# Optimization experiments

Measured on AMD Instinct MI355X. Metric: run time of the kernel, lower is better.

Reference implementation:

```python
import jax, jax.numpy as jnp
import numpy as np

# ---- fan-beam geometry config (uniform path: no pmatrix, uniform SID/SDD/angle/offcenter) ----
SID = 750.0          # source-to-isocenter distance (mm)
SDD = 1250.0         # source-to-detector distance (mm)
VIEWS = 128          # number of projection angles
NDET = 512           # detector element count
DET_ELT = 1.2        # detector element size (mm)
DET_OFF = 0.0        # detector offcenter (mm)
START_ANGLE = 0.0    # degrees
TOTAL_ANGLE = 360.0  # degrees
IMG_DIM = 256        # image is IMG_DIM x IMG_DIM
PIX = 1.0            # pixel size (mm)
STEP = 1.0           # fpjStepSize: ray sampling step (mm)
R = IMG_DIM * PIX * np.sqrt(2.0) / 2.0   # half image diagonal: ray segment to sample
NS = int(np.ceil(2.0 * R / STEP)) + 1    # samples per ray (static)


def _sample_points():
    # Per-view source / detector geometry; rays sampled from t = SID-R to SID+R.
    beta = jnp.asarray(np.deg2rad(START_ANGLE + TOTAL_ANGLE * np.arange(VIEWS) / VIEWS),
                       jnp.float32)                                    # [V]
    cb, sb = jnp.cos(beta), jnp.sin(beta)
    src = SID * jnp.stack([cb, sb], -1)                                 # [V,2] source position
    det0 = src - SDD * jnp.stack([cb, sb], -1)                          # [V,2] detector center
    eu = jnp.stack([-sb, cb], -1)                                       # [V,2] detector tangent
    u = (jnp.arange(NDET, dtype=jnp.float32) - (NDET - 1) / 2.0) * DET_ELT + DET_OFF  # [N]
    det = det0[:, None, :] + u[None, :, None] * eu[:, None, :]          # [V,N,2]
    d = det - src[:, None, :]
    d = d / jnp.linalg.norm(d, axis=-1, keepdims=True)                  # unit ray directions
    t = SID - R + STEP * jnp.arange(NS, dtype=jnp.float32)              # [NS]
    pts = src[:, None, None, :] + t[None, None, :, None] * d[:, :, None, :]  # [V,N,NS,2]
    return pts


def setup_inputs() -> dict:
    key = jax.random.key(0)
    x = jax.random.uniform(key, (2, IMG_DIM, IMG_DIM), dtype=jnp.float32)  # attenuation image batch
    return {"x": x}


def reference(x):
    # Ray-driven fan-beam forward projection: line integral via bilinear sampling.
    pts = _sample_points()                      # [V,N,NS,2] world coords (mm)
    px, py = pts[..., 0], pts[..., 1]
    jx = px / PIX + (IMG_DIM - 1) / 2.0         # continuous column index
    iy = (IMG_DIM - 1) / 2.0 - py / PIX         # continuous row index (y up)
    j0f = jnp.floor(jx)
    i0f = jnp.floor(iy)
    fj = jx - j0f
    fi = iy - i0f
    i0 = i0f.astype(jnp.int32)
    j0 = j0f.astype(jnp.int32)

    def gather(ii, jj):
        valid = (ii >= 0) & (ii < IMG_DIM) & (jj >= 0) & (jj < IMG_DIM)
        ic = jnp.clip(ii, 0, IMG_DIM - 1)
        jc = jnp.clip(jj, 0, IMG_DIM - 1)
        return x[:, ic, jc] * valid[None].astype(x.dtype)   # [B,V,N,NS]

    v00 = gather(i0, j0)
    v01 = gather(i0, j0 + 1)
    v10 = gather(i0 + 1, j0)
    v11 = gather(i0 + 1, j0 + 1)
    interp = (v00 * (1 - fi) * (1 - fj) + v01 * (1 - fi) * fj
              + v10 * fi * (1 - fj) + v11 * fi * fj)        # [B,V,N,NS]
    sinogram = interp.sum(-1) * STEP                        # [B,V,N]
    return sinogram
```

## Files before the change

kernel.cpp:

```cpp
#include <hip/hip_runtime.h>
#include <hip/hip_fp16.h>
#include <math.h>
#include <string.h>

constexpr int   VIEWS = 128;
constexpr int   NDET  = 512;
constexpr int   IMG   = 256;
constexpr int   BATCH = 2;
constexpr float SID_F = 750.0f;
constexpr float SDD_F = 1250.0f;
constexpr float DET_ELT = 1.2f;
constexpr float DET_OFF = 0.0f;
constexpr float STEP  = 1.0f;
constexpr int   NS = 364;
constexpr float T0 = (float)(750.0 - 181.01933598375618);

constexpr int PAD    = 2;
constexpr int TROWS  = IMG + 2 * PAD;
constexpr int TSTR   = 262;
constexpr int TWSTR  = TSTR / 2;
constexpr int TWORDS = TROWS * TWSTR;

typedef _Float16 h2 __attribute__((ext_vector_type(2)));
using v2h = decltype(__builtin_amdgcn_cvt_pkrtz(0.0f, 0.0f));

__global__ __launch_bounds__(1024) void fanbeam_lds(const float* __restrict__ img,
                                                    float* __restrict__ out) {
    __shared__ unsigned int tile32[TWORDS];
    __shared__ float red[1024];
    const int tid = threadIdx.x;
    const int blk = blockIdx.x;
    const int v = blk & (VIEWS - 1);
    const int b = blk >> 7;

    for (int k = tid; k < 524 + 768; k += 1024) {
        int w;
        if (k < 524) {
            const int r = k / 131, c = k - r * 131;
            const int row = (r < 2) ? r : 256 + r;
            w = row * TWSTR + c;
        } else {
            const int kk = k - 524;
            const int row = 2 + kk / 3;
            const int m = kk % 3;
            w = row * TWSTR + ((m == 0) ? 0 : 128 + m);
        }
        tile32[w] = 0u;
    }

    const float* __restrict__ src = img + b * IMG * IMG;
    for (int k = tid; k < (IMG * IMG) / 4; k += 1024) {
        const int p = k * 4;
        const int i = p >> 8;
        const int j = p & 255;
        const float4 f = *reinterpret_cast<const float4*>(src + p);
        const unsigned lo = ((unsigned)__half_as_ushort(__float2half(f.y)) << 16)
                          |  (unsigned)__half_as_ushort(__float2half(f.x));
        const unsigned hi = ((unsigned)__half_as_ushort(__float2half(f.w)) << 16)
                          |  (unsigned)__half_as_ushort(__float2half(f.z));
        const int h = (i + PAD) * TSTR + (j + PAD);
        tile32[h >> 1]       = lo;
        tile32[(h >> 1) + 1] = hi;
    }
    __syncthreads();

    const int n     = tid & (NDET - 1);
    const int chunk = tid >> 9;
    const float beta = (float)((double)v * 0.049087385212340517);
    const float cb = cosf(beta);
    const float sb = sinf(beta);
    const float u  = ((float)n - 255.5f) * DET_ELT + DET_OFF;
    float dx = fmaf(-u, sb, -SDD_F * cb);
    float dy = fmaf( u, cb, -SDD_F * sb);
    const float inv = rsqrtf(fmaf(dx, dx, dy * dy));
    dx *= inv;
    dy *= inv;
    const float ndy = -dy;
    const float sx = SID_F * cb;
    const float sy = SID_F * sb;
    const float cx3 = fmaf(T0, dx,  sx + 127.5f + (float)PAD);
    const float cy3 = fmaf(T0, ndy, 127.5f - sy + (float)PAD);

    const float invx = 1.0f / dx;
    const float invy = 1.0f / dy;
    const float ta = (-128.75f - sx) * invx, tb = (128.75f - sx) * invx;
    const float tc = (-128.75f - sy) * invy, td = (128.75f - sy) * invy;
    const float txmin = fminf(ta, tb), txmax = fmaxf(ta, tb);
    const float tymin = fminf(tc, td), tymax = fmaxf(tc, td);
    const float tmin = fmaxf(fmaxf(txmin, tymin), T0);
    const float tmax = fminf(fminf(txmax, tymax), T0 + (float)(NS - 1));
    int slo = (int)ceilf(tmin - T0);
    int shi = (int)floorf(tmax - T0);
    slo = max(slo, 0);
    shi = min(shi, NS - 1);

    float acc = 0.0f;
    const int start = slo + chunk;
    const int iters = max(0, (shi - start + 2) / 2);
    float sfv = (float)start;

#pragma unroll 4
    for (int k = 0; k < iters; ++k) {
        const float jx2 = fmaf(sfv, dx, cx3);
        const float iy2 = fmaf(sfv, ndy, cy3);
        sfv += 2.0f;
        const int jp = (int)jx2;
        const int ip = (int)iy2;
        const float fj = jx2 - (float)jp;
        const float fi = iy2 - (float)ip;
        const int w = ip * TWSTR + (jp >> 1);
        const unsigned w0 = tile32[w];
        const unsigned w1 = tile32[w + 1];
        const unsigned w2 = tile32[w + TWSTR];
        const unsigned w3 = tile32[w + TWSTR + 1];
        const unsigned sh = (unsigned)jp << 4;
        const unsigned ptop = __builtin_amdgcn_alignbit(w1, w0, sh);
        const unsigned pbot = __builtin_amdgcn_alignbit(w3, w2, sh);
        const unsigned Lu = __builtin_amdgcn_perm(pbot, ptop, 0x05040100u);
        const unsigned Hu = __builtin_amdgcn_perm(pbot, ptop, 0x07060302u);
        const h2 L = __builtin_bit_cast(h2, Lu);
        const h2 H = __builtin_bit_cast(h2, Hu);
        const h2 fj2 = __builtin_bit_cast(h2, __builtin_amdgcn_cvt_pkrtz(fj, fj));
        const h2 r = fj2 * (H - L) + L;
#if __has_builtin(__builtin_amdgcn_fdot2)
        const h2 wv = __builtin_bit_cast(h2, __builtin_amdgcn_cvt_pkrtz(1.0f - fi, fi));
        acc = __builtin_amdgcn_fdot2(__builtin_bit_cast(v2h, r),
                                     __builtin_bit_cast(v2h, wv), acc, false);
#else
        const float top = (float)r.x;
        const float bot = (float)r.y;
        acc = fmaf(fi, bot - top, acc + top);
#endif
    }

    red[tid] = acc;
    __syncthreads();
    if (tid < 512) {
        out[blk * 512 + tid] = (red[tid] + red[tid + 512]) * STEP;
    }
}

extern "C" void kernel_launch(void* const* d_in, const int* in_sizes, int n_in,
                              void* d_out, int out_size, void* d_ws, size_t ws_size,
                              hipStream_t stream) {
    const float* x = (const float*)d_in[0];
    float* out = (float*)d_out;
    fanbeam_lds<<<BATCH * VIEWS, 1024, 0, stream>>>(x, out);
}
```

Before: 77.02 us.

## Store vertically paired fp16 texels and process image in two row bands

Changes the LDS layout so each 32-bit word holds a pixel and the one below it. A bilinear sample then needs two LDS reads instead of four, and the alignbit/perm unpacking goes away. The doubled tile no longer fits for the whole image, so the image is loaded in two overlapping row bands, and each ray's sample range is split at the band boundary. The cost is a second tile load with scalar, uncoalesced-width global reads and fp16 conversion, plus extra barriers. Block-level memory-load latency is also no longer overlapped.

```diff
diff --git a/kernel.cpp b/kernel.cpp
--- a/kernel.cpp
+++ b/kernel.cpp
@@ -1,7 +1,6 @@
 #include <hip/hip_runtime.h>
 #include <hip/hip_fp16.h>
 #include <math.h>
-#include <string.h>
 
 constexpr int   VIEWS = 128;
 constexpr int   NDET  = 512;
@@ -15,54 +14,60 @@
 constexpr int   NS = 364;
 constexpr float T0 = (float)(750.0 - 181.01933598375618);
 
-constexpr int PAD    = 2;
-constexpr int TROWS  = IMG + 2 * PAD;
-constexpr int TSTR   = 262;
-constexpr int TWSTR  = TSTR / 2;
-constexpr int TWORDS = TROWS * TWSTR;
+constexpr int COLS  = 260;
+constexpr int CSTR  = 261;
+constexpr int SPLIT = 130;
+constexpr int NE_T  = 131;
+constexpr int NE_B  = 130;
+constexpr int BLO_B = 129;
 
 typedef _Float16 h2 __attribute__((ext_vector_type(2)));
 using v2h = decltype(__builtin_amdgcn_cvt_pkrtz(0.0f, 0.0f));
 
-__global__ __launch_bounds__(1024) void fanbeam_lds(const float* __restrict__ img,
-                                                    float* __restrict__ out) {
-    __shared__ unsigned int tile32[TWORDS];
+__device__ __forceinline__ float band_loop(const unsigned* __restrict__ tb,
+                                           int lo, int hi, int chunk,
+                                           float dx, float ndy,
+                                           float cx3, float cy3) {
+    float acc = 0.0f;
+    const int start = lo + chunk;
+    const int iters = max(0, (hi - start + 2) / 2);
+    float sfv = (float)start;
+#pragma unroll 4
+    for (int k = 0; k < iters; ++k) {
+        const float jx2 = fmaf(sfv, dx, cx3);
+        const float iy2 = fmaf(sfv, ndy, cy3);
+        sfv += 2.0f;
+        const int jp = (int)jx2;
+        const int ip = (int)iy2;
+        const float fj = jx2 - (float)jp;
+        const float fi = iy2 - (float)ip;
+        const int addr = ip * CSTR + jp;
+        const unsigned Lu = tb[addr];
+        const unsigned Hu = tb[addr + 1];
+        const h2 L = __builtin_bit_cast(h2, Lu);
+        const h2 H = __builtin_bit_cast(h2, Hu);
+        const h2 fj2 = __builtin_bit_cast(h2, __builtin_amdgcn_cvt_pkrtz(fj, fj));
+        const h2 r = fj2 * (H - L) + L;
+#if __has_builtin(__builtin_amdgcn_fdot2)
+        const h2 wv = __builtin_bit_cast(h2, __builtin_amdgcn_cvt_pkrtz(1.0f - fi, fi));
+        acc = __builtin_amdgcn_fdot2(__builtin_bit_cast(v2h, r),
+                                     __builtin_bit_cast(v2h, wv), acc, false);
+#else
+        acc = fmaf(fi, (float)r.y - (float)r.x, acc + (float)r.x);
+#endif
+    }
+    return acc;
+}
+
+__global__ __launch_bounds__(1024) void fanbeam_pair(const float* __restrict__ img,
+                                                     float* __restrict__ out) {
+    __shared__ unsigned tile[NE_T * CSTR];
     __shared__ float red[1024];
     const int tid = threadIdx.x;
     const int blk = blockIdx.x;
     const int v = blk & (VIEWS - 1);
     const int b = blk >> 7;
-
-    for (int k = tid; k < 524 + 768; k += 1024) {
-        int w;
-        if (k < 524) {
-            const int r = k / 131, c = k - r * 131;
-            const int row = (r < 2) ? r : 256 + r;
-            w = row * TWSTR + c;
-        } else {
-            const int kk = k - 524;
-            const int row = 2 + kk / 3;
-            const int m = kk % 3;
-            w = row * TWSTR + ((m == 0) ? 0 : 128 + m);
-        }
-        tile32[w] = 0u;
-    }
-
     const float* __restrict__ src = img + b * IMG * IMG;
-    for (int k = tid; k < (IMG * IMG) / 4; k += 1024) {
-        const int p = k * 4;
-        const int i = p >> 8;
-        const int j = p & 255;
-        const float4 f = *reinterpret_cast<const float4*>(src + p);
-        const unsigned lo = ((unsigned)__half_as_ushort(__float2half(f.y)) << 16)
-                          |  (unsigned)__half_as_ushort(__float2half(f.x));
-        const unsigned hi = ((unsigned)__half_as_ushort(__float2half(f.w)) << 16)
-                          |  (unsigned)__half_as_ushort(__float2half(f.z));
-        const int h = (i + PAD) * TSTR + (j + PAD);
-        tile32[h >> 1]       = lo;
-        tile32[(h >> 1) + 1] = hi;
-    }
-    __syncthreads();
 
     const int n     = tid & (NDET - 1);
     const int chunk = tid >> 9;
@@ -72,68 +77,74 @@
     const float u  = ((float)n - 255.5f) * DET_ELT + DET_OFF;
     float dx = fmaf(-u, sb, -SDD_F * cb);
     float dy = fmaf( u, cb, -SDD_F * sb);
-    const float inv = rsqrtf(fmaf(dx, dx, dy * dy));
-    dx *= inv;
-    dy *= inv;
+    const float rinv = rsqrtf(fmaf(dx, dx, dy * dy));
+    dx *= rinv;
+    dy *= rinv;
     const float ndy = -dy;
     const float sx = SID_F * cb;
     const float sy = SID_F * sb;
-    const float cx3 = fmaf(T0, dx,  sx + 127.5f + (float)PAD);
-    const float cy3 = fmaf(T0, ndy, 127.5f - sy + (float)PAD);
+    const float cx3 = fmaf(T0, dx,  sx + 127.5f + 2.0f);
+    const float cy3 = fmaf(T0, ndy, 127.5f - sy + 2.0f);
 
     const float invx = 1.0f / dx;
     const float invy = 1.0f / dy;
-    const float ta = (-128.75f - sx) * invx, tb = (128.75f - sx) * invx;
+    const float ta = (-128.75f - sx) * invx, tb2 = (128.75f - sx) * invx;
     const float tc = (-128.75f - sy) * invy, td = (128.75f - sy) * invy;
-    const float txmin = fminf(ta, tb), txmax = fmaxf(ta, tb);
-    const float tymin = fminf(tc, td), tymax = fmaxf(tc, td);
-    const float tmin = fmaxf(fmaxf(txmin, tymin), T0);
-    const float tmax = fminf(fminf(txmax, tymax), T0 + (float)(NS - 1));
+    const float tmin = fmaxf(fmaxf(fminf(ta, tb2), fminf(tc, td)), T0);
+    const float tmax = fminf(fminf(fmaxf(ta, tb2), fmaxf(tc, td)), T0 + (float)(NS - 1));
     int slo = (int)ceilf(tmin - T0);
     int shi = (int)floorf(tmax - T0);
     slo = max(slo, 0);
     shi = min(shi, NS - 1);
 
-    float acc = 0.0f;
-    const int start = slo + chunk;
-    const int iters = max(0, (shi - start + 2) / 2);
-    float sfv = (float)start;
+    float zf = (cy3 - (float)SPLIT) * invy;
+    zf = fminf(fmaxf(zf, -1.0e6f), 1.0e6f);
+    const int zc  = (int)ceilf(zf);
+    const int zfl = (int)floorf(zf);
 
-#pragma unroll 4
-    for (int k = 0; k < iters; ++k) {
-        const float jx2 = fmaf(sfv, dx, cx3);
-        const float iy2 = fmaf(sfv, ndy, cy3);
-        sfv += 2.0f;
-        const int jp = (int)jx2;
-        const int ip = (int)iy2;
-        const float fj = jx2 - (float)jp;
-        const float fi = iy2 - (float)ip;
-        const int w = ip * TWSTR + (jp >> 1);
-        const unsigned w0 = tile32[w];
-        const unsigned w1 = tile32[w + 1];
-        const unsigned w2 = tile32[w + TWSTR];
-        const unsigned w3 = tile32[w + TWSTR + 1];
-        const unsigned sh = (unsigned)jp << 4;
-        const unsigned ptop = __builtin_amdgcn_alignbit(w1, w0, sh);
-        const unsigned pbot = __builtin_amdgcn_alignbit(w3, w2, sh);
-        const unsigned Lu = __builtin_amdgcn_perm(pbot, ptop, 0x05040100u);
-        const unsigned Hu = __builtin_amdgcn_perm(pbot, ptop, 0x07060302u);
-        const h2 L = __builtin_bit_cast(h2, Lu);
-        const h2 H = __builtin_bit_cast(h2, Hu);
-        const h2 fj2 = __builtin_bit_cast(h2, __builtin_amdgcn_cvt_pkrtz(fj, fj));
-        const h2 r = fj2 * (H - L) + L;
-#if __has_builtin(__builtin_amdgcn_fdot2)
-        const h2 wv = __builtin_bit_cast(h2, __builtin_amdgcn_cvt_pkrtz(1.0f - fi, fi));
-        acc = __builtin_amdgcn_fdot2(__builtin_bit_cast(v2h, r),
-                                     __builtin_bit_cast(v2h, wv), acc, false);
-#else
-        const float top = (float)r.x;
-        const float bot = (float)r.y;
-        acc = fmaf(fi, bot - top, acc + top);
-#endif
+    for (int k = tid; k < NE_T * COLS; k += 1024) {
+        const int e = k / COLS;
+        const int j = k - e * COLS;
+        const int r0 = e - 2, r1 = e - 1, c = j - 2;
+        const bool cv = (unsigned)c < 256u;
+        unsigned plo = 0, phi = 0;
+        if (cv && (unsigned)r0 < 256u)
+            plo = __half_as_ushort(__float2half(src[(r0 << 8) + c]));
+        if (cv && (unsigned)r1 < 256u)
+            phi = __half_as_ushort(__float2half(src[(r1 << 8) + c]));
+        tile[e * CSTR + j] = plo | (phi << 16);
     }
+    __syncthreads();
+    int lo_, hi_;
+    if (ndy > 0.0f)      { lo_ = slo; hi_ = min(shi, zc - 1); }
+    else if (ndy < 0.0f) { lo_ = max(slo, zfl + 1); hi_ = shi; }
+    else                 { lo_ = (cy3 < (float)SPLIT) ? slo : 1;
+                           hi_ = (cy3 < (float)SPLIT) ? shi : 0; }
+    const float accT = band_loop(tile, lo_, hi_, chunk, dx, ndy, cx3, cy3);
+    __syncthreads();
 
-    red[tid] = acc;
+    for (int k = tid; k < NE_B * COLS; k += 1024) {
+        const int e = k / COLS;
+        const int j = k - e * COLS;
+        const int p = e + BLO_B;
+        const int r0 = p - 2, r1 = p - 1, c = j - 2;
+        const bool cv = (unsigned)c < 256u;
+        unsigned plo = 0, phi = 0;
+        if (cv && (unsigned)r0 < 256u)
+            plo = __half_as_ushort(__float2half(src[(r0 << 8) + c]));
+        if (cv && (unsigned)r1 < 256u)
+            phi = __half_as_ushort(__float2half(src[(r1 << 8) + c]));
+        tile[e * CSTR + j] = plo | (phi << 16);
+    }
+    __syncthreads();
+    if (ndy > 0.0f)      { lo_ = max(slo, zc); hi_ = shi; }
+    else if (ndy < 0.0f) { lo_ = slo; hi_ = min(shi, zfl); }
+    else                 { lo_ = (cy3 < (float)SPLIT) ? 1 : slo;
+                           hi_ = (cy3 < (float)SPLIT) ? 0 : shi; }
+    const float accB = band_loop(tile - BLO_B * CSTR, lo_, hi_, chunk,
+                                 dx, ndy, cx3, cy3);
+
+    red[tid] = accT + accB;
     __syncthreads();
     if (tid < 512) {
         out[blk * 512 + tid] = (red[tid] + red[tid + 512]) * STEP;
@@ -145,5 +156,5 @@
                               hipStream_t stream) {
     const float* x = (const float*)d_in[0];
     float* out = (float*)d_out;
-    fanbeam_lds<<<BATCH * VIEWS, 1024, 0, stream>>>(x, out);
+    fanbeam_pair<<<BATCH * VIEWS, 1024, 0, stream>>>(x, out);
 }
```

Measured after the change: 104.7 us. 1.36x slower.
